# Performance work log

Hardware: AMD Instinct MI355X
Metric: run time of the kernel (lower is better)

The kernel has to match this reference:

```python
import jax, jax.numpy as jnp
import numpy as np

D_MODEL = 1024
D_INNER = 2048
D_STATE = 16
D_CONV = 4
DT_RANK = 64
BATCH = 2
SEQ = 1024


def _silu(v):
    return v * jax.nn.sigmoid(v)


def setup_inputs() -> dict:
    key = jax.random.key(0)
    ks = jax.random.split(key, 8)
    s = 0.02
    return {
        "x": jax.random.normal(ks[0], (BATCH, SEQ, D_MODEL), jnp.float32),
        "norm_w": jnp.ones((D_MODEL,), jnp.float32),
        "in_proj_w": (jax.random.normal(ks[1], (2 * D_INNER, D_MODEL), jnp.float32) * s),
        "conv_w": (jax.random.normal(ks[2], (D_INNER, 1, D_CONV), jnp.float32) * s),
        "conv_b": jnp.zeros((D_INNER,), jnp.float32),
        "x_proj_w": (jax.random.normal(ks[3], (DT_RANK + 2 * D_STATE, D_INNER), jnp.float32) * s),
        "dt_proj_w": (jax.random.normal(ks[4], (D_INNER, DT_RANK), jnp.float32) * s),
        "dt_proj_b": jnp.zeros((D_INNER,), jnp.float32),
        "A_log": jnp.log(jnp.broadcast_to(jnp.arange(1, D_STATE + 1, dtype=jnp.float32), (D_INNER, D_STATE))),
        "D": jnp.ones((D_INNER,), jnp.float32),
        "out_proj_w": (jax.random.normal(ks[5], (D_MODEL, D_INNER), jnp.float32) * s),
    }


def reference(x, norm_w, in_proj_w, conv_w, conv_b, x_proj_w, dt_proj_w, dt_proj_b, A_log, D, out_proj_w):
    b, l, d = x.shape
    x_copy = x
    # MambaRMSNorm
    h = x * jax.lax.rsqrt(jnp.mean(x * x, axis=-1, keepdims=True) + 1e-5) * norm_w
    # in_proj -> split into x-path and residual gate
    x_and_res = h @ in_proj_w.T                       # [b, l, 2*d_inner]
    xs, res = jnp.split(x_and_res, 2, axis=-1)
    # causal depthwise conv1d (torch pads d_conv-1 both sides then slices [:l])
    xc = jnp.transpose(xs, (0, 2, 1))                 # [b, d_inner, l]
    xc = jax.lax.conv_general_dilated(
        xc, conv_w, window_strides=(1,), padding=[(D_CONV - 1, 0)],
        feature_group_count=D_INNER, dimension_numbers=("NCH", "OIH", "NCH"))
    xc = xc + conv_b[None, :, None]
    u = _silu(jnp.transpose(xc, (0, 2, 1)))           # [b, l, d_inner]
    # SSM parameters
    A = -jnp.exp(A_log)                               # [d_inner, n]
    x_dbl = u @ x_proj_w.T                            # [b, l, dt_rank + 2n]
    delta, Bm, Cm = jnp.split(x_dbl, [DT_RANK, DT_RANK + D_STATE], axis=-1)
    delta = jax.nn.softplus(delta @ dt_proj_w.T + dt_proj_b)   # [b, l, d_inner]
    deltaA = jnp.exp(jnp.einsum("bld,dn->bldn", delta, A))     # [b, l, d_inner, n]
    deltaB_u = (delta * u)[..., None] * Bm[:, :, None, :]      # [b, l, d_inner, n]

    def step(state, inp):
        dA, dBu, c = inp                               # [b,d,n],[b,d,n],[b,n]
        state = dA * state + dBu
        y = jnp.einsum("bdn,bn->bd", state, c)
        return state, y

    init = jnp.zeros((b, D_INNER, D_STATE), dtype=u.dtype)
    _, ys = jax.lax.scan(
        step, init,
        (jnp.transpose(deltaA, (1, 0, 2, 3)),
         jnp.transpose(deltaB_u, (1, 0, 2, 3)),
         jnp.transpose(Cm, (1, 0, 2))))
    y = jnp.transpose(ys, (1, 0, 2)) + u * D           # [b, l, d_inner]
    y = y * _silu(res)
    return y @ out_proj_w.T + x_copy
```

## Files before the change

### kernel.cpp

```cpp
#include <hip/hip_runtime.h>
#include <hip/hip_bf16.h>
#include <math.h>

constexpr int B_   = 2;
constexpr int L_   = 1024;
constexpr int DM   = 1024;
constexpr int DI   = 2048;
constexpr int NS   = 16;
constexpr int DTR  = 64;
constexpr int TOK  = B_ * L_;
constexpr int NC   = 32;

typedef __attribute__((ext_vector_type(8))) short short8;
typedef __attribute__((ext_vector_type(4))) float f32x4;
using bf16 = __hip_bfloat16;

__device__ __forceinline__ float sigmoidf_(float v) {
    return 1.f / (1.f + __expf(-v));
}
__device__ __forceinline__ float softplusf_(float v) {
    return fmaxf(v, 0.f) + __logf(1.f + __expf(-fabsf(v)));
}

__device__ __forceinline__ f32x4 mfma16(short8 a, short8 b, f32x4 c) {
    return __builtin_amdgcn_mfma_f32_16x16x32_bf16(a, b, c, 0, 0, 0);
}

__global__ __launch_bounds__(256) void k_rmsnorm(
    const float* __restrict__ x, const float* __restrict__ w,
    bf16* __restrict__ hh, bf16* __restrict__ hl)
{
    int row = blockIdx.x;
    const float4* xrp = (const float4*)(x + (size_t)row * DM);
    float4 v = xrp[threadIdx.x];
    float ss = v.x*v.x + v.y*v.y + v.z*v.z + v.w*v.w;
    #pragma unroll
    for (int m = 32; m >= 1; m >>= 1) ss += __shfl_xor(ss, m);
    __shared__ float acc[4];
    int wid = threadIdx.x >> 6, lane = threadIdx.x & 63;
    if (lane == 0) acc[wid] = ss;
    __syncthreads();
    float tot = acc[0] + acc[1] + acc[2] + acc[3];
    float sc = rsqrtf(tot * (1.f / DM) + 1e-5f);
    float4 wv = ((const float4*)w)[threadIdx.x];
    float o[4] = { v.x*sc*wv.x, v.y*sc*wv.y, v.z*sc*wv.z, v.w*sc*wv.w };
    alignas(8) bf16 H[4], Lo[4];
    #pragma unroll
    for (int j = 0; j < 4; ++j) {
        H[j]  = __float2bfloat16(o[j]);
        Lo[j] = __float2bfloat16(o[j] - __bfloat162float(H[j]));
    }
    size_t base = (size_t)row * DM + threadIdx.x * 4;
    *(ushort4*)(hh + base) = *(ushort4*)H;
    *(ushort4*)(hl + base) = *(ushort4*)Lo;
}

__global__ __launch_bounds__(256) void k_split(
    const float* __restrict__ s, bf16* __restrict__ hi, bf16* __restrict__ lo, int n4)
{
    int i = blockIdx.x * 256 + threadIdx.x;
    if (i >= n4) return;
    float4 v = ((const float4*)s)[i];
    float f[4] = { v.x, v.y, v.z, v.w };
    alignas(8) bf16 H[4], Lo[4];
    #pragma unroll
    for (int j = 0; j < 4; ++j) {
        H[j]  = __float2bfloat16(f[j]);
        Lo[j] = __float2bfloat16(f[j] - __bfloat162float(H[j]));
    }
    *(ushort4*)(hi + (size_t)i * 4) = *(ushort4*)H;
    *(ushort4*)(lo + (size_t)i * 4) = *(ushort4*)Lo;
}

__global__ __launch_bounds__(256) void k_split_pad(
    const float* __restrict__ s, bf16* __restrict__ hi, bf16* __restrict__ lo)
{
    int i = blockIdx.x * 256 + threadIdx.x;
    int row = i >> 9;
    float f[4] = {0.f, 0.f, 0.f, 0.f};
    if (row < 96) {
        float4 v = ((const float4*)s)[i];
        f[0] = v.x; f[1] = v.y; f[2] = v.z; f[3] = v.w;
    }
    alignas(8) bf16 H[4], Lo[4];
    #pragma unroll
    for (int j = 0; j < 4; ++j) {
        H[j]  = __float2bfloat16(f[j]);
        Lo[j] = __float2bfloat16(f[j] - __bfloat162float(H[j]));
    }
    *(ushort4*)(hi + (size_t)i * 4) = *(ushort4*)H;
    *(ushort4*)(lo + (size_t)i * 4) = *(ushort4*)Lo;
}

__global__ __launch_bounds__(128) void k_xdbl_post(
    const float* __restrict__ xdbl, bf16* __restrict__ hi, bf16* __restrict__ lo,
    float* __restrict__ bc_t)
{
    int tok = blockIdx.x, col = threadIdx.x;
    if (col >= 96) return;
    float v = xdbl[(size_t)tok * 96 + col];
    bf16 H = __float2bfloat16(v);
    hi[(size_t)tok * 96 + col] = H;
    lo[(size_t)tok * 96 + col] = __float2bfloat16(v - __bfloat162float(H));
    if (col >= 64) bc_t[(size_t)(col - 64) * TOK + tok] = v;
}

__device__ __forceinline__ void stage_tile(const bf16* src, int ld, bf16* lds, int lane)
{
    #pragma unroll
    for (int j = 0; j < 8; ++j) {
        int c = (j << 6) + lane;
        int r = c >> 2;
        int g = (c & 3) ^ ((r >> 1) & 3);
        __builtin_amdgcn_global_load_lds(
            (const __attribute__((address_space(1))) unsigned int*)(src + (size_t)r * ld + (g << 3)),
            (__attribute__((address_space(3))) unsigned int*)(lds + (j << 9)),
            16, 0, 0);
    }
}

template<int NA, int EPI>
__global__ __launch_bounds__(256) void k_gemm_bf16(
    const bf16* __restrict__ Ah, const bf16* __restrict__ Al, int lda,
    const bf16* __restrict__ Bh, const bf16* __restrict__ Bl, int ldb,
    float* __restrict__ C, int ldc,
    const float* __restrict__ aux,
    int M, int Nb, int Kc)
{
    __shared__ alignas(1024) bf16 sA[2][NA][128 * 32];
    __shared__ alignas(1024) bf16 sB[2][2][128 * 32];

    int tid = threadIdx.x, lane = tid & 63, wv = tid >> 6;
    int bm0 = blockIdx.y * 128, bn0 = blockIdx.x * 128;
    int kbase = blockIdx.z * Kc;
    int nkt = Kc >> 5;

    const bf16* Abase_h = Ah + (size_t)bm0 * lda + kbase;
    const bf16* Abase_l = (NA == 2) ? (Al + (size_t)bm0 * lda + kbase) : nullptr;
    const bf16* Bbase_h = Bh + (size_t)bn0 * ldb + kbase;
    const bf16* Bbase_l = Bl + (size_t)bn0 * ldb + kbase;

    auto stage_all = [&](int buf, int kt) {
        int k0 = kt << 5;
        if constexpr (NA == 2) {
            if      (wv == 0) stage_tile(Abase_h + k0, lda, &sA[buf][0][0], lane);
            else if (wv == 1) stage_tile(Abase_l + k0, lda, &sA[buf][1][0], lane);
            else if (wv == 2) stage_tile(Bbase_h + k0, ldb, &sB[buf][0][0], lane);
            else              stage_tile(Bbase_l + k0, ldb, &sB[buf][1][0], lane);
        } else {
            if      (wv == 0) stage_tile(Abase_h + k0, lda, &sA[buf][0][0], lane);
            else if (wv == 1) stage_tile(Bbase_h + k0, ldb, &sB[buf][0][0], lane);
            else if (wv == 2) stage_tile(Bbase_l + k0, ldb, &sB[buf][1][0], lane);
        }
    };
    auto frag = [&](const bf16* t, int r, int g) -> short8 {
        int c = (r << 2) + (g ^ ((r >> 1) & 3));
        return *(const short8*)(t + (c << 3));
    };

    int wr = (wv >> 1) << 6;
    int wc = (wv & 1) << 6;
    int fr = lane & 15, g = lane >> 4;

    f32x4 acc[4][4] = {};

    stage_all(0, 0);
    __syncthreads();
    for (int kt = 0; kt < nkt; ++kt) {
        int cur = kt & 1;
        if (kt + 1 < nkt) stage_all(cur ^ 1, kt + 1);
        short8 a0[4], a1[4], b0[4], b1[4];
        #pragma unroll
        for (int m = 0; m < 4; ++m) {
            a0[m] = frag(&sA[cur][0][0], wr + m * 16 + fr, g);
            if constexpr (NA == 2) a1[m] = frag(&sA[cur][NA - 1][0], wr + m * 16 + fr, g);
        }
        #pragma unroll
        for (int n = 0; n < 4; ++n) {
            b0[n] = frag(&sB[cur][0][0], wc + n * 16 + fr, g);
            b1[n] = frag(&sB[cur][1][0], wc + n * 16 + fr, g);
        }
        #pragma unroll
        for (int m = 0; m < 4; ++m)
            #pragma unroll
            for (int n = 0; n < 4; ++n) {
                acc[m][n] = mfma16(a0[m], b0[n], acc[m][n]);
                acc[m][n] = mfma16(a0[m], b1[n], acc[m][n]);
                if constexpr (NA == 2) acc[m][n] = mfma16(a1[m], b0[n], acc[m][n]);
            }
        __syncthreads();
    }

    int rbase = bm0 + wr + (g << 2);
    int cb = bn0 + wc + fr;
    if constexpr (EPI == 4) {
        #pragma unroll
        for (int m = 0; m < 4; ++m)
            #pragma unroll
            for (int n = 0; n < 4; ++n) {
                int col = cb + n * 16;
                float b_ = aux[col];
                float vv[4];
                #pragma unroll
                for (int i = 0; i < 4; ++i)
                    vv[i] = softplusf_(acc[m][n][i] + b_);
                *(float4*)&C[(size_t)col * ldc + rbase + m * 16] = *(float4*)vv;
            }
    } else {
        #pragma unroll
        for (int m = 0; m < 4; ++m)
            #pragma unroll
            for (int i = 0; i < 4; ++i) {
                int row = rbase + m * 16 + i;
                #pragma unroll
                for (int n = 0; n < 4; ++n) {
                    int col = cb + n * 16;
                    float v = acc[m][n][i];
                    if constexpr (EPI == 3) {
                        if (col < Nb) atomicAdd(&C[(size_t)row * ldc + col], v);
                    } else {
                        if constexpr (EPI == 1) v = softplusf_(v + aux[col]);
                        if constexpr (EPI == 2) v += aux[(size_t)row * ldc + col];
                        C[(size_t)row * ldc + col] = v;
                    }
                }
            }
    }
}

__global__ __launch_bounds__(256) void k_conv_silu(
    const float* __restrict__ xr, const float* __restrict__ w,
    const float* __restrict__ bconv,
    bf16* __restrict__ uh, bf16* __restrict__ ul, float* __restrict__ u_t)
{
    int idx = blockIdx.x * 256 + threadIdx.x;
    int dq = idx & 511;
    int ts = idx >> 9;
    int bb = ts >> 7;
    int t0 = (ts & 127) * 8;
    int dd = dq * 4;

    float4 wrow[4];
    #pragma unroll
    for (int j = 0; j < 4; j++)
        wrow[j] = *(const float4*)&w[(dd + j) * 4];
    float4 bias4 = *(const float4*)&bconv[dd];
    const float bias_[4] = { bias4.x, bias4.y, bias4.z, bias4.w };

    auto ldrow = [&](int t) -> float4 {
        if (t < 0) return make_float4(0.f, 0.f, 0.f, 0.f);
        return *(const float4*)&xr[((size_t)(bb * L_ + t)) * (2 * DI) + dd];
    };
    float4 a = ldrow(t0 - 3), b = ldrow(t0 - 2), c = ldrow(t0 - 1);

    float uout[4][8];
    #pragma unroll
    for (int k = 0; k < 8; ++k) {
        float4 d4 = ldrow(t0 + k);
        const float as[4] = {a.x, a.y, a.z, a.w};
        const float bs[4] = {b.x, b.y, b.z, b.w};
        const float cs[4] = {c.x, c.y, c.z, c.w};
        const float ds[4] = {d4.x, d4.y, d4.z, d4.w};
        alignas(8) bf16 H[4], Lo[4];
        #pragma unroll
        for (int j = 0; j < 4; ++j) {
            const float* wj = (const float*)&wrow[j];
            float acc = bias_[j];
            acc = fmaf(as[j], wj[0], acc);
            acc = fmaf(bs[j], wj[1], acc);
            acc = fmaf(cs[j], wj[2], acc);
            acc = fmaf(ds[j], wj[3], acc);
            float o = acc * sigmoidf_(acc);
            uout[j][k] = o;
            H[j]  = __float2bfloat16(o);
            Lo[j] = __float2bfloat16(o - __bfloat162float(H[j]));
        }
        size_t base = ((size_t)(bb * L_ + t0 + k)) * DI + dd;
        *(ushort4*)(uh + base) = *(ushort4*)H;
        *(ushort4*)(ul + base) = *(ushort4*)Lo;
        a = b; b = c; c = d4;
    }
    #pragma unroll
    for (int j = 0; j < 4; ++j) {
        size_t tb = (size_t)(dd + j) * TOK + bb * L_ + t0;
        *(float4*)&u_t[tb]     = make_float4(uout[j][0], uout[j][1], uout[j][2], uout[j][3]);
        *(float4*)&u_t[tb + 4] = make_float4(uout[j][4], uout[j][5], uout[j][6], uout[j][7]);
    }
}

__global__ __launch_bounds__(256) void k_scan_part(
    const float* __restrict__ delta_t, const float* __restrict__ u_t,
    const float* __restrict__ bc_t,    const float* __restrict__ A_log,
    float* __restrict__ P, float* __restrict__ S)
{
    int bx = blockIdx.x;
    int c = bx & (NC - 1);
    int rest = bx >> 5;
    int b = rest >> 5;
    int d0 = (rest & 31) << 6;
    int t = threadIdx.x;
    int dl_ = t >> 2, q = t & 3;
    int d = d0 + dl_;

    float A_dn[4];
    #pragma unroll
    for (int j = 0; j < 4; ++j)
        A_dn[j] = -__expf(A_log[d * NS + q * 4 + j]);

    float s[4] = {};
    float dsum = 0.f;
    int tokb = b * L_ + c * (L_ / NC);
    const float* dbase = delta_t + (size_t)d * TOK + tokb;
    const float* ubase = u_t + (size_t)d * TOK + tokb;
    const float* Bbase = bc_t + (size_t)(q * 4) * TOK + tokb;

    for (int g = 0; g < (L_ / NC) / 4; ++g) {
        float4 dl4 = *(const float4*)(dbase + g * 4);
        float4 uu4 = *(const float4*)(ubase + g * 4);
        float Bm_[4][4];
        #pragma unroll
        for (int j = 0; j < 4; ++j) {
            float4 bv = *(const float4*)(Bbase + (size_t)j * TOK + g * 4);
            Bm_[j][0] = bv.x; Bm_[j][1] = bv.y; Bm_[j][2] = bv.z; Bm_[j][3] = bv.w;
        }
        const float dls[4] = {dl4.x, dl4.y, dl4.z, dl4.w};
        const float uus[4] = {uu4.x, uu4.y, uu4.z, uu4.w};
        #pragma unroll
        for (int k = 0; k < 4; ++k) {
            float dlu = dls[k] * uus[k];
            dsum += dls[k];
            #pragma unroll
            for (int j = 0; j < 4; ++j) {
                float e = __expf(dls[k] * A_dn[j]);
                s[j] = fmaf(e, s[j], dlu * Bm_[j][k]);
            }
        }
    }
    float p[4];
    #pragma unroll
    for (int j = 0; j < 4; ++j)
        p[j] = __expf(A_dn[j] * dsum);
    size_t o = (((size_t)(b * NC + c) * DI) + d) * NS + q * 4;
    *(float4*)&P[o] = *(float4*)p;
    *(float4*)&S[o] = *(float4*)s;
}

__global__ __launch_bounds__(256) void k_scan_comb(
    const float* __restrict__ P, float* __restrict__ S)
{
    int idx = blockIdx.x * 256 + threadIdx.x;
    int n = idx & 15;
    int d = (idx >> 4) & (DI - 1);
    int b = idx >> 15;
    float carry = 0.f;
    #pragma unroll
    for (int c = 0; c < NC; ++c) {
        size_t o = (((size_t)(b * NC + c) * DI) + d) * NS + n;
        float Pv = P[o], Sv = S[o];
        S[o] = carry;
        carry = fmaf(Pv, carry, Sv);
    }
}

__global__ __launch_bounds__(256) void k_scan_y(
    const float* __restrict__ delta_t, const float* __restrict__ u_t,
    const float* __restrict__ bc_t,    const float* __restrict__ xr,
    const float* __restrict__ A_log,   const float* __restrict__ Dp,
    const float* __restrict__ init, bf16* __restrict__ y)
{
    int bx = blockIdx.x;
    int c = bx & (NC - 1);
    int rest = bx >> 5;
    int b = rest >> 5;
    int d0 = (rest & 31) << 6;
    int t = threadIdx.x;
    int dl_ = t >> 2, q = t & 3;
    int d = d0 + dl_;

    float A_dn[4];
    #pragma unroll
    for (int j = 0; j < 4; ++j)
        A_dn[j] = -__expf(A_log[d * NS + q * 4 + j]);
    float Dd = Dp[d];

    size_t o = (((size_t)(b * NC + c) * DI) + d) * NS + q * 4;
    float4 s4 = *(const float4*)&init[o];
    float s[4] = {s4.x, s4.y, s4.z, s4.w};

    int tokb = b * L_ + c * (L_ / NC);
    const float* dbase = delta_t + (size_t)d * TOK + tokb;
    const float* ubase = u_t + (size_t)d * TOK + tokb;
    const float* Bbase = bc_t + (size_t)(q * 4) * TOK + tokb;
    const float* Cbase = bc_t + (size_t)(16 + q * 4) * TOK + tokb;

    for (int g = 0; g < (L_ / NC) / 4; ++g) {
        int tok0 = tokb + g * 4;
        float4 dl4 = *(const float4*)(dbase + g * 4);
        float4 uu4 = *(const float4*)(ubase + g * 4);
        float Bm_[4][4], Cm_[4][4];
        #pragma unroll
        for (int j = 0; j < 4; ++j) {
            float4 bv = *(const float4*)(Bbase + (size_t)j * TOK + g * 4);
            float4 cv = *(const float4*)(Cbase + (size_t)j * TOK + g * 4);
            Bm_[j][0] = bv.x; Bm_[j][1] = bv.y; Bm_[j][2] = bv.z; Bm_[j][3] = bv.w;
            Cm_[j][0] = cv.x; Cm_[j][1] = cv.y; Cm_[j][2] = cv.z; Cm_[j][3] = cv.w;
        }
        const float dls[4] = {dl4.x, dl4.y, dl4.z, dl4.w};
        const float uus[4] = {uu4.x, uu4.y, uu4.z, uu4.w};
        float py[4];
        #pragma unroll
        for (int k = 0; k < 4; ++k) {
            float dlu = dls[k] * uus[k];
            float a_ = 0.f;
            #pragma unroll
            for (int j = 0; j < 4; ++j) {
                float e = __expf(dls[k] * A_dn[j]);
                s[j] = fmaf(e, s[j], dlu * Bm_[j][k]);
                a_ = fmaf(s[j], Cm_[j][k], a_);
            }
            py[k] = a_;
        }
        #pragma unroll
        for (int k = 0; k < 4; ++k) {
            py[k] += __shfl_xor(py[k], 1);
            py[k] += __shfl_xor(py[k], 2);
        }
        float py_q = py[0], uu_q = uus[0];
        py_q = (q == 1) ? py[1] : py_q;  uu_q = (q == 1) ? uus[1] : uu_q;
        py_q = (q == 2) ? py[2] : py_q;  uu_q = (q == 2) ? uus[2] : uu_q;
        py_q = (q == 3) ? py[3] : py_q;  uu_q = (q == 3) ? uus[3] : uu_q;
        int tok = tok0 + q;
        float rr = xr[(size_t)tok * (2 * DI) + DI + d];
        float yv = fmaf(uu_q, Dd, py_q) * (rr * sigmoidf_(rr));
        y[(size_t)tok * DI + d] = __float2bfloat16(yv);
    }
}

extern "C" void kernel_launch(void* const* d_in, const int* in_sizes, int n_in,
                              void* d_out, int out_size, void* d_ws, size_t ws_size,
                              hipStream_t stream)
{
    const float* x       = (const float*)d_in[0];
    const float* norm_w  = (const float*)d_in[1];
    const float* in_proj = (const float*)d_in[2];
    const float* conv_w  = (const float*)d_in[3];
    const float* conv_b  = (const float*)d_in[4];
    const float* x_proj  = (const float*)d_in[5];
    const float* dt_w    = (const float*)d_in[6];
    const float* dt_b    = (const float*)d_in[7];
    const float* A_log   = (const float*)d_in[8];
    const float* Dp      = (const float*)d_in[9];
    const float* out_w   = (const float*)d_in[10];
    float* out = (float*)d_out;

    constexpr size_t MB = 1u << 20;
    constexpr size_t KB = 1u << 10;
    char* Wb = (char*)d_ws;
    float* xr      = (float*)(Wb + 0);
    bf16*  h_h     = (bf16*) (Wb + 32 * MB);
    bf16*  h_l     = (bf16*) (Wb + 36 * MB);
    bf16*  u_h     = (bf16*) (Wb + 32 * MB);
    bf16*  u_l     = (bf16*) (Wb + 40 * MB);
    float* Pbuf    = (float*)(Wb + 32 * MB);
    float* Sbuf    = (float*)(Wb + 40 * MB);
    bf16*  y_h     = (bf16*) (Wb + 32 * MB);
    float* u_t     = (float*)(Wb + 48 * MB);
    bf16*  wo_h    = (bf16*) (Wb + 48 * MB);
    bf16*  wo_l    = (bf16*) (Wb + 52 * MB);
    bf16*  wi_h    = (bf16*) (Wb + 64 * MB);
    bf16*  wi_l    = (bf16*) (Wb + 72 * MB);
    float* delta_t = (float*)(Wb + 64 * MB);
    float* xdbl    = (float*)(Wb + 80 * MB);
    bf16*  xp_h    = (bf16*) (Wb + 80 * MB + 768 * KB);
    bf16*  xp_l    = (bf16*) (Wb + 81 * MB + 256 * KB);
    bf16*  xdbl_h  = (bf16*) (Wb + 81 * MB + 768 * KB);
    bf16*  xdbl_l  = (bf16*) (Wb + 82 * MB + 128 * KB);
    float* bc_t    = (float*)(Wb + 82 * MB + 512 * KB);
    bf16*  dtw_h   = (bf16*) (Wb + 82 * MB + 768 * KB);
    bf16*  dtw_l   = (bf16*) (Wb + 83 * MB);

    k_rmsnorm<<<TOK, 256, 0, stream>>>(x, norm_w, h_h, h_l);
    k_split<<<4096, 256, 0, stream>>>(in_proj, wi_h, wi_l, (2 * DI * DM) / 4);
    k_gemm_bf16<2, 0><<<dim3(32, 16, 1), 256, 0, stream>>>(
        h_h, h_l, DM, wi_h, wi_l, DM, xr, 2 * DI, nullptr, TOK, 2 * DI, DM);
    k_conv_silu<<<512, 256, 0, stream>>>(xr, conv_w, conv_b, u_h, u_l, u_t);
    k_split_pad<<<256, 256, 0, stream>>>(x_proj, xp_h, xp_l);
    hipMemsetAsync(xdbl, 0, (size_t)TOK * 96 * sizeof(float), stream);
    k_gemm_bf16<2, 3><<<dim3(1, 16, 32), 256, 0, stream>>>(
        u_h, u_l, DI, xp_h, xp_l, DI, xdbl, 96, nullptr, TOK, 96, DI / 32);
    k_xdbl_post<<<TOK, 128, 0, stream>>>(xdbl, xdbl_h, xdbl_l, bc_t);
    k_split<<<128, 256, 0, stream>>>(dt_w, dtw_h, dtw_l, (DI * DTR) / 4);
    k_gemm_bf16<2, 4><<<dim3(16, 16, 1), 256, 0, stream>>>(
        xdbl_h, xdbl_l, 96, dtw_h, dtw_l, DTR, delta_t, TOK, dt_b, TOK, DI, DTR);
    k_scan_part<<<B_ * NC * (DI / 64), 256, 0, stream>>>(
        delta_t, u_t, bc_t, A_log, Pbuf, Sbuf);
    k_scan_comb<<<256, 256, 0, stream>>>(Pbuf, Sbuf);
    k_scan_y<<<B_ * NC * (DI / 64), 256, 0, stream>>>(
        delta_t, u_t, bc_t, xr, A_log, Dp, Sbuf, y_h);
    k_split<<<2048, 256, 0, stream>>>(out_w, wo_h, wo_l, (DM * DI) / 4);
    hipMemcpyAsync(out, x, (size_t)TOK * DM * sizeof(float),
                   hipMemcpyDeviceToDevice, stream);
    k_gemm_bf16<1, 3><<<dim3(8, 16, 4), 256, 0, stream>>>(
        y_h, nullptr, DI, wo_h, wo_l, DI, out, DM, nullptr, TOK, DM, DI / 4);
}
```

Before: 368.2 us.

## Replace atomic split-K with partial buffers and reduction kernels; merge weight splits

The split-K GEMMs for x_proj and out_proj now write per-slice partial tiles into workspace buffers instead of using atomicAdd. Dedicated reduce kernels sum the slices. The x_proj reduce also produces the bf16 hi/lo halves and the transposed B/C, and the out_proj reduce adds the residual, which removes a memset and a device-to-device copy. The three weight hi/lo split kernels are merged into one launch, and the x_proj split-K factor drops from 32 to 16. This trades atomic contention and extra launches for additional partial-buffer traffic: for out_proj that is four full-size fp32 partials written and read back.

```diff
diff --git a/kernel.cpp b/kernel.cpp
--- a/kernel.cpp
+++ b/kernel.cpp
@@ -10,6 +10,8 @@
 constexpr int DTR  = 64;
 constexpr int TOK  = B_ * L_;
 constexpr int NC   = 32;
+constexpr int ZX   = 16;
+constexpr int ZO   = 4;
 
 typedef __attribute__((ext_vector_type(8))) short short8;
 typedef __attribute__((ext_vector_type(4))) float f32x4;
@@ -72,37 +74,68 @@
     *(ushort4*)(lo + (size_t)i * 4) = *(ushort4*)Lo;
 }
 
-__global__ __launch_bounds__(256) void k_split_pad(
-    const float* __restrict__ s, bf16* __restrict__ hi, bf16* __restrict__ lo)
+constexpr int N4_WI  = (2 * DI * DM) / 4;
+constexpr int N4_DTW = (DI * DTR) / 4;
+constexpr int N4_XP  = (128 * DI) / 4;
+__global__ __launch_bounds__(256) void k_split_all(
+    const float* __restrict__ wi, const float* __restrict__ dtw,
+    const float* __restrict__ xp,
+    bf16* __restrict__ wi_h, bf16* __restrict__ wi_l,
+    bf16* __restrict__ dtw_h, bf16* __restrict__ dtw_l,
+    bf16* __restrict__ xp_h, bf16* __restrict__ xp_l)
 {
     int i = blockIdx.x * 256 + threadIdx.x;
-    int row = i >> 9;
+    const float* src; bf16 *hi, *lo; int j; bool zero = false;
+    if (i < N4_WI)                  { j = i;                    src = wi;  hi = wi_h;  lo = wi_l; }
+    else if (i < N4_WI + N4_DTW)    { j = i - N4_WI;            src = dtw; hi = dtw_h; lo = dtw_l; }
+    else if (i < N4_WI + N4_DTW + N4_XP) {
+        j = i - N4_WI - N4_DTW; src = xp; hi = xp_h; lo = xp_l;
+        zero = (j >> 9) >= 96;
+    } else return;
     float f[4] = {0.f, 0.f, 0.f, 0.f};
-    if (row < 96) {
-        float4 v = ((const float4*)s)[i];
+    if (!zero) {
+        float4 v = ((const float4*)src)[j];
         f[0] = v.x; f[1] = v.y; f[2] = v.z; f[3] = v.w;
     }
     alignas(8) bf16 H[4], Lo[4];
     #pragma unroll
-    for (int j = 0; j < 4; ++j) {
-        H[j]  = __float2bfloat16(f[j]);
-        Lo[j] = __float2bfloat16(f[j] - __bfloat162float(H[j]));
-    }
-    *(ushort4*)(hi + (size_t)i * 4) = *(ushort4*)H;
-    *(ushort4*)(lo + (size_t)i * 4) = *(ushort4*)Lo;
-}
-
-__global__ __launch_bounds__(128) void k_xdbl_post(
-    const float* __restrict__ xdbl, bf16* __restrict__ hi, bf16* __restrict__ lo,
+    for (int k = 0; k < 4; ++k) {
+        H[k]  = __float2bfloat16(f[k]);
+        Lo[k] = __float2bfloat16(f[k] - __bfloat162float(H[k]));
+    }
+    *(ushort4*)(hi + (size_t)j * 4) = *(ushort4*)H;
+    *(ushort4*)(lo + (size_t)j * 4) = *(ushort4*)Lo;
+}
+
+__global__ __launch_bounds__(192) void k_xdbl_reduce(
+    const float* __restrict__ part, bf16* __restrict__ hi, bf16* __restrict__ lo,
     float* __restrict__ bc_t)
 {
-    int tok = blockIdx.x, col = threadIdx.x;
-    if (col >= 96) return;
-    float v = xdbl[(size_t)tok * 96 + col];
+    int t = threadIdx.x;
+    int tok = blockIdx.x * 2 + (t >= 96 ? 1 : 0);
+    int col = (t >= 96) ? t - 96 : t;
+    float v = 0.f;
+    #pragma unroll
+    for (int z = 0; z < ZX; ++z)
+        v += part[((size_t)z * TOK + tok) * 96 + col];
     bf16 H = __float2bfloat16(v);
     hi[(size_t)tok * 96 + col] = H;
     lo[(size_t)tok * 96 + col] = __float2bfloat16(v - __bfloat162float(H));
     if (col >= 64) bc_t[(size_t)(col - 64) * TOK + tok] = v;
+}
+
+__global__ __launch_bounds__(256) void k_out_reduce(
+    const float* __restrict__ part, const float* __restrict__ x,
+    float* __restrict__ out)
+{
+    int i = blockIdx.x * 256 + threadIdx.x;
+    float4 a = ((const float4*)x)[i];
+    #pragma unroll
+    for (int z = 0; z < ZO; ++z) {
+        float4 p = ((const float4*)(part + (size_t)z * TOK * DM))[i];
+        a.x += p.x; a.y += p.y; a.z += p.z; a.w += p.w;
+    }
+    ((float4*)out)[i] = a;
 }
 
 __device__ __forceinline__ void stage_tile(const bf16* src, int ld, bf16* lds, int lane)
@@ -206,7 +239,8 @@
                     vv[i] = softplusf_(acc[m][n][i] + b_);
                 *(float4*)&C[(size_t)col * ldc + rbase + m * 16] = *(float4*)vv;
             }
-    } else {
+    } else if constexpr (EPI == 5) {
+        float* Cz = C + (size_t)blockIdx.z * M * Nb;
         #pragma unroll
         for (int m = 0; m < 4; ++m)
             #pragma unroll
@@ -215,15 +249,19 @@
                 #pragma unroll
                 for (int n = 0; n < 4; ++n) {
                     int col = cb + n * 16;
-                    float v = acc[m][n][i];
-                    if constexpr (EPI == 3) {
-                        if (col < Nb) atomicAdd(&C[(size_t)row * ldc + col], v);
-                    } else {
-                        if constexpr (EPI == 1) v = softplusf_(v + aux[col]);
-                        if constexpr (EPI == 2) v += aux[(size_t)row * ldc + col];
-                        C[(size_t)row * ldc + col] = v;
-                    }
+                    if (col < Nb)
+                        Cz[(size_t)row * Nb + col] = acc[m][n][i];
                 }
+            }
+    } else {
+        #pragma unroll
+        for (int m = 0; m < 4; ++m)
+            #pragma unroll
+            for (int i = 0; i < 4; ++i) {
+                int row = rbase + m * 16 + i;
+                #pragma unroll
+                for (int n = 0; n < 4; ++n)
+                    C[(size_t)row * ldc + cb + n * 16] = acc[m][n][i];
             }
     }
 }
@@ -464,32 +502,31 @@
     float* Pbuf    = (float*)(Wb + 32 * MB);
     float* Sbuf    = (float*)(Wb + 40 * MB);
     bf16*  y_h     = (bf16*) (Wb + 32 * MB);
+    bf16*  wo_h    = (bf16*) (Wb + 40 * MB);
+    bf16*  wo_l    = (bf16*) (Wb + 44 * MB);
     float* u_t     = (float*)(Wb + 48 * MB);
-    bf16*  wo_h    = (bf16*) (Wb + 48 * MB);
-    bf16*  wo_l    = (bf16*) (Wb + 52 * MB);
+    float* out_prt = (float*)(Wb + 48 * MB);
     bf16*  wi_h    = (bf16*) (Wb + 64 * MB);
     bf16*  wi_l    = (bf16*) (Wb + 72 * MB);
+    float* xp_prt  = (float*)(Wb + 64 * MB);
     float* delta_t = (float*)(Wb + 64 * MB);
-    float* xdbl    = (float*)(Wb + 80 * MB);
-    bf16*  xp_h    = (bf16*) (Wb + 80 * MB + 768 * KB);
-    bf16*  xp_l    = (bf16*) (Wb + 81 * MB + 256 * KB);
-    bf16*  xdbl_h  = (bf16*) (Wb + 81 * MB + 768 * KB);
-    bf16*  xdbl_l  = (bf16*) (Wb + 82 * MB + 128 * KB);
-    float* bc_t    = (float*)(Wb + 82 * MB + 512 * KB);
-    bf16*  dtw_h   = (bf16*) (Wb + 82 * MB + 768 * KB);
-    bf16*  dtw_l   = (bf16*) (Wb + 83 * MB);
+    bf16*  xp_h    = (bf16*) (Wb + 80 * MB);
+    bf16*  xp_l    = (bf16*) (Wb + 80 * MB + 512 * KB);
+    bf16*  xdbl_h  = (bf16*) (Wb + 81 * MB);
+    bf16*  xdbl_l  = (bf16*) (Wb + 81 * MB + 384 * KB);
+    float* bc_t    = (float*)(Wb + 81 * MB + 768 * KB);
+    bf16*  dtw_h   = (bf16*) (Wb + 82 * MB);
+    bf16*  dtw_l   = (bf16*) (Wb + 82 * MB + 256 * KB);
 
     k_rmsnorm<<<TOK, 256, 0, stream>>>(x, norm_w, h_h, h_l);
-    k_split<<<4096, 256, 0, stream>>>(in_proj, wi_h, wi_l, (2 * DI * DM) / 4);
+    k_split_all<<<(N4_WI + N4_DTW + N4_XP + 255) / 256, 256, 0, stream>>>(
+        in_proj, dt_w, x_proj, wi_h, wi_l, dtw_h, dtw_l, xp_h, xp_l);
     k_gemm_bf16<2, 0><<<dim3(32, 16, 1), 256, 0, stream>>>(
         h_h, h_l, DM, wi_h, wi_l, DM, xr, 2 * DI, nullptr, TOK, 2 * DI, DM);
     k_conv_silu<<<512, 256, 0, stream>>>(xr, conv_w, conv_b, u_h, u_l, u_t);
-    k_split_pad<<<256, 256, 0, stream>>>(x_proj, xp_h, xp_l);
-    hipMemsetAsync(xdbl, 0, (size_t)TOK * 96 * sizeof(float), stream);
-    k_gemm_bf16<2, 3><<<dim3(1, 16, 32), 256, 0, stream>>>(
-        u_h, u_l, DI, xp_h, xp_l, DI, xdbl, 96, nullptr, TOK, 96, DI / 32);
-    k_xdbl_post<<<TOK, 128, 0, stream>>>(xdbl, xdbl_h, xdbl_l, bc_t);
-    k_split<<<128, 256, 0, stream>>>(dt_w, dtw_h, dtw_l, (DI * DTR) / 4);
+    k_gemm_bf16<2, 5><<<dim3(1, 16, ZX), 256, 0, stream>>>(
+        u_h, u_l, DI, xp_h, xp_l, DI, xp_prt, 96, nullptr, TOK, 96, DI / ZX);
+    k_xdbl_reduce<<<TOK / 2, 192, 0, stream>>>(xp_prt, xdbl_h, xdbl_l, bc_t);
     k_gemm_bf16<2, 4><<<dim3(16, 16, 1), 256, 0, stream>>>(
         xdbl_h, xdbl_l, 96, dtw_h, dtw_l, DTR, delta_t, TOK, dt_b, TOK, DI, DTR);
     k_scan_part<<<B_ * NC * (DI / 64), 256, 0, stream>>>(
@@ -498,8 +535,7 @@
     k_scan_y<<<B_ * NC * (DI / 64), 256, 0, stream>>>(
         delta_t, u_t, bc_t, xr, A_log, Dp, Sbuf, y_h);
     k_split<<<2048, 256, 0, stream>>>(out_w, wo_h, wo_l, (DM * DI) / 4);
-    hipMemcpyAsync(out, x, (size_t)TOK * DM * sizeof(float),
-                   hipMemcpyDeviceToDevice, stream);
-    k_gemm_bf16<1, 3><<<dim3(8, 16, 4), 256, 0, stream>>>(
-        y_h, nullptr, DI, wo_h, wo_l, DI, out, DM, nullptr, TOK, DM, DI / 4);
-}
+    k_gemm_bf16<1, 5><<<dim3(8, 16, ZO), 256, 0, stream>>>(
+        y_h, nullptr, DI, wo_h, wo_l, DI, out_prt, DM, nullptr, TOK, DM, DI / ZO);
+    k_out_reduce<<<TOK * DM / 4 / 256, 256, 0, stream>>>(out_prt, x, out);
+}
```

Result: faster. 335.6 us (-8.8%).
